# Kernel tuning notes

Hardware: AMD Instinct MI355X
Metric: run time of the kernel (lower is better)

## Reference

```python
import jax, jax.numpy as jnp
import numpy as np

B, H, S = 2048, 1024, 128


def setup_inputs() -> dict:
    key = jax.random.key(0)
    ks = jax.random.split(key, 8)
    s = 0.05  # keep gates out of saturation, roughly 1/sqrt(H) init scale
    return {
        "hidden": jax.random.normal(ks[0], (1, B, H), jnp.float32) * s,
        "cell": jax.random.normal(ks[1], (1, B, H), jnp.float32) * s,
        "W_ih": jax.random.normal(ks[2], (4 * H, 1), jnp.float32) * s,
        "W_hh": jax.random.normal(ks[3], (4 * H, H), jnp.float32) * s,
        "b_ih": jax.random.normal(ks[4], (4 * H,), jnp.float32) * s,
        "b_hh": jax.random.normal(ks[5], (4 * H,), jnp.float32) * s,
        "W_fc": jax.random.normal(ks[6], (S, H), jnp.float32) * s,
        "b_fc": jax.random.normal(ks[7], (S,), jnp.float32) * s,
    }


def reference(hidden, cell, W_ih, W_hh, b_ih, b_hh, W_fc, b_fc):
    # prediction from per-step head fc_i fed back as next input.
    h0 = hidden[0]  # [B, H] (num_layers = 1)
    c0 = cell[0]
    b = b_ih + b_hh  # [4H]
    x0 = jnp.zeros((h0.shape[0], 1), h0.dtype)  # initial zero input [B, 1]

    def step(carry, fc_t):
        h, c, x = carry
        Wt, bt = fc_t  # Wt: [H], bt: scalar
        gates = x @ W_ih.T + h @ W_hh.T + b  # [B, 4H], torch gate order i,f,g,o
        i, f, g, o = jnp.split(gates, 4, axis=-1)
        c = jax.nn.sigmoid(f) * c + jax.nn.sigmoid(i) * jnp.tanh(g)
        h = jax.nn.sigmoid(o) * jnp.tanh(c)
        pred = h @ Wt + bt  # [B] (Linear(H,1) then squeeze)
        return (h, c, pred[:, None]), pred

    _, preds = jax.lax.scan(step, (h0, c0, x0), (W_fc, b_fc))  # preds: [S, B]
    return preds.T  # [B, S]
```

## Files before the change

kernel.cpp:

```cpp
#include <hip/hip_runtime.h>
#include <hip/hip_bf16.h>
#include <stdint.h>

#define B_SZ 2048
#define H_SZ 1024
#define S_SZ 128
#define G4   4096
#define BK   64
#define NKK  (H_SZ / BK)

typedef short short8 __attribute__((ext_vector_type(8)));
typedef float floatx4 __attribute__((ext_vector_type(4)));

#define AS1 __attribute__((address_space(1)))
#define AS3 __attribute__((address_space(3)))

__device__ ushort g_Wp[G4 * H_SZ];
__device__ ushort g_h[2][B_SZ * H_SZ];
__device__ float  g_c[B_SZ * H_SZ];
__device__ float  g_wih[G4];
__device__ float  g_bias[G4];
__device__ float  g_pp[2][32][B_SZ];

__device__ __forceinline__ float bf2f(ushort u) {
  return __uint_as_float(((unsigned)u) << 16);
}
__device__ __forceinline__ ushort f2bf(float f) {
  unsigned u = __float_as_uint(f);
  return (ushort)((u + 0x7FFFu + ((u >> 16) & 1u)) >> 16);
}
__device__ __forceinline__ float fsig(float x) { return 1.f / (1.f + __expf(-x)); }
__device__ __forceinline__ float ftanh(float x) { return 1.f - 2.f / (__expf(2.f * x) + 1.f); }

__device__ __forceinline__ void gload16(const void* g, void* l) {
  __builtin_amdgcn_global_load_lds((const AS1 void*)g, (AS3 void*)l, 16, 0, 0);
}


__global__ __launch_bounds__(256) void prep_wpack(const float* __restrict__ Whh) {
  const int gid = blockIdx.x * 256 + threadIdx.x;
  const int j   = gid >> 7;
  const int k8  = (gid & 127) << 3;
  const int gate = (j >> 4) & 3;
  const int h    = ((j >> 6) << 4) | (j & 15);
  const float* src = Whh + (size_t)(gate * H_SZ + h) * H_SZ + k8;
  floatx4 a = *(const floatx4*)src;
  floatx4 b = *(const floatx4*)(src + 4);
  short8 o;
#pragma unroll
  for (int i = 0; i < 4; ++i) o[i] = (short)f2bf(a[i]);
#pragma unroll
  for (int i = 0; i < 4; ++i) o[4 + i] = (short)f2bf(b[i]);
  *(short8*)&g_Wp[(size_t)j * H_SZ + (k8 ^ ((j & 7) << 3))] = o;
}

__global__ __launch_bounds__(256) void prep_misc(const float* __restrict__ Wih,
                                                 const float* __restrict__ bih,
                                                 const float* __restrict__ bhh) {
  const int j = blockIdx.x * 256 + threadIdx.x;
  const int gate = (j >> 4) & 3;
  const int h    = ((j >> 6) << 4) | (j & 15);
  const int jp   = gate * H_SZ + h;
  g_wih[j]  = Wih[jp];
  g_bias[j] = bih[jp] + bhh[jp];
}

__global__ __launch_bounds__(256) void prep_state(const float* __restrict__ hidden,
                                                  const float* __restrict__ cell) {
  const int gid = blockIdx.x * 256 + threadIdx.x;
  const int row = gid >> 7;
  const int k8  = (gid & 127) << 3;
  const size_t src = (size_t)row * H_SZ + k8;
  short8 o;
#pragma unroll
  for (int i = 0; i < 8; ++i) o[i] = (short)f2bf(hidden[src + i]);
  *(short8*)&g_h[0][(size_t)row * H_SZ + (k8 ^ ((row & 7) << 3))] = o;
  floatx4 c0 = *(const floatx4*)&cell[src];
  floatx4 c1 = *(const floatx4*)&cell[src + 4];
  *(floatx4*)&g_c[src]     = c0;
  *(floatx4*)&g_c[src + 4] = c1;
}

__global__ __launch_bounds__(256, 2)
void lstm_step(int t, int p, const float* __restrict__ Wfc,
               const float* __restrict__ bfc, float* __restrict__ out) {
  __shared__ ushort Al[2][128 * BK];
  __shared__ ushort Bl[2][128 * BK];

  const ushort* __restrict__ hin = g_h[p];
  ushort* __restrict__ hout      = g_h[p ^ 1];

  const int tid  = threadIdx.x;
  const int lane = tid & 63;
  const int wid  = tid >> 6;
  const int bid  = blockIdx.x;
  const int xcd  = bid & 7;
  const int idx  = bid >> 3;
  const int jt   = (xcd << 2) | (idx & 3);
  const int bt   = idx >> 2;
  const int brow = bt << 7;
  const int jcol = jt << 7;
  const int wr = wid >> 1, wc = wid & 1;
  const int lr = lane & 15, lk = lane >> 4;
  const int xorv = (lr & 7) << 3;

  const int srow = lane >> 3;
  const int scol = (lane & 7) << 3;
  const size_t arb = (size_t)(brow + wid * 32 + srow) * H_SZ + scol;
  const size_t brb = (size_t)(jcol + wid * 32 + srow) * H_SZ + scol;
  ushort* const ad0 = &Al[0][wid * 32 * BK];
  ushort* const ad1 = &Al[1][wid * 32 * BK];
  ushort* const bd0 = &Bl[0][wid * 32 * BK];
  ushort* const bd1 = &Bl[1][wid * 32 * BK];

  floatx4 acc[4][4];
#pragma unroll
  for (int m = 0; m < 4; ++m)
#pragma unroll
    for (int n = 0; n < 4; ++n) acc[m][n] = {0.f, 0.f, 0.f, 0.f};

  int aoff[4], boff[4];
#pragma unroll
  for (int m = 0; m < 4; ++m) aoff[m] = (wr * 64 + m * 16 + lr) * BK;
#pragma unroll
  for (int n = 0; n < 4; ++n) boff[n] = (wc * 64 + n * 16 + lr) * BK;
  const int c0 = (lk * 8) ^ xorv;
  const int c1 = (32 + lk * 8) ^ xorv;

#define STAGE(AD, BD, KO)                                                   \
  {                                                                         \
    const int ko_ = (KO) * BK;                                              \
    _Pragma("unroll") for (int i = 0; i < 4; ++i) {                         \
      gload16(hin + arb + (size_t)i * 8 * H_SZ + ko_, AD + i * 8 * BK);     \
      gload16(g_Wp + brb + (size_t)i * 8 * H_SZ + ko_, BD + i * 8 * BK);    \
    }                                                                       \
  }

#define COMPUTE(AC, BC)                                                     \
  {                                                                         \
    short8 a[4], b[4];                                                      \
    _Pragma("unroll") for (int k2 = 0; k2 < 2; ++k2) {                      \
      const int cc_ = k2 ? c1 : c0;                                         \
      _Pragma("unroll") for (int m = 0; m < 4; ++m)                         \
          a[m] = *(const short8*)&(AC)[aoff[m] + cc_];                      \
      _Pragma("unroll") for (int n = 0; n < 4; ++n)                         \
          b[n] = *(const short8*)&(BC)[boff[n] + cc_];                      \
      _Pragma("unroll") for (int m = 0; m < 4; ++m)                         \
          _Pragma("unroll") for (int n = 0; n < 4; ++n)                     \
              acc[m][n] = __builtin_amdgcn_mfma_f32_16x16x32_bf16(          \
                  a[m], b[n], acc[m][n], 0, 0, 0);                          \
    }                                                                       \
  }

  STAGE(ad0, bd0, 0);
  __syncthreads();

  for (int kk = 0; kk < NKK; kk += 2) {
    STAGE(ad1, bd1, kk + 1);
    COMPUTE(Al[0], Bl[0]);
    __syncthreads();
    if (kk + 2 < NKK) STAGE(ad0, bd0, kk + 2);
    COMPUTE(Al[1], Bl[1]);
    __syncthreads();
  }

  float* predp = (float*)&Al[0][0];
  float* xbuf  = (float*)&Bl[0][0];

  if (t > 0 && tid < 128) {
    float s = 0.f;
#pragma unroll
    for (int j = 0; j < 32; ++j) s += g_pp[(t - 1) & 1][j][brow + tid];
    s += bfc[t - 1];
    xbuf[tid] = s;
    if (jt == 0) out[(size_t)(brow + tid) * S_SZ + (t - 1)] = s;
  }
  __syncthreads();

  const int hcol = ((jt * 2 + wc) << 4) + lr;
  const float wfc_l = Wfc[(size_t)t * H_SZ + hcol];
  float wih[4], bb[4];
#pragma unroll
  for (int n = 0; n < 4; ++n) {
    const int col = jcol + wc * 64 + n * 16 + lr;
    wih[n] = g_wih[col];
    bb[n]  = g_bias[col];
  }

#pragma unroll
  for (int m = 0; m < 4; ++m) {
#pragma unroll
    for (int r = 0; r < 4; ++r) {
      const int row_l = wr * 64 + m * 16 + lk * 4 + r;
      const float xv = (t > 0) ? xbuf[row_l] : 0.f;
      float gi = acc[m][0][r] + xv * wih[0] + bb[0];
      float gf = acc[m][1][r] + xv * wih[1] + bb[1];
      float gg = acc[m][2][r] + xv * wih[2] + bb[2];
      float go = acc[m][3][r] + xv * wih[3] + bb[3];
      const int row = brow + row_l;
      const size_t cidx = (size_t)row * H_SZ + hcol;
      float cc = g_c[cidx];
      float cn = fsig(gf) * cc + fsig(gi) * ftanh(gg);
      g_c[cidx] = cn;
      float hv = fsig(go) * ftanh(cn);
      hout[(size_t)row * H_SZ + (hcol ^ ((row_l & 7) << 3))] = f2bf(hv);
      float pp = hv * wfc_l;
      pp += __shfl_xor(pp, 1);
      pp += __shfl_xor(pp, 2);
      pp += __shfl_xor(pp, 4);
      pp += __shfl_xor(pp, 8);
      if (lr == 0) predp[wc * 128 + row_l] = pp;
    }
  }
  __syncthreads();
  if (tid < 128) g_pp[t & 1][jt][brow + tid] = predp[tid] + predp[128 + tid];
#undef STAGE
#undef COMPUTE
}

__global__ __launch_bounds__(256)
void pred_last(const float* __restrict__ bfc, float* __restrict__ out) {
  const int row = blockIdx.x * 256 + threadIdx.x;
  float s = 0.f;
#pragma unroll
  for (int j = 0; j < 32; ++j) s += g_pp[1][j][row];
  out[(size_t)row * S_SZ + (S_SZ - 1)] = s + bfc[S_SZ - 1];
}

extern "C" void kernel_launch(void* const* d_in, const int* in_sizes, int n_in,
                              void* d_out, int out_size, void* d_ws, size_t ws_size,
                              hipStream_t stream) {
  const float* hidden = (const float*)d_in[0];
  const float* cell   = (const float*)d_in[1];
  const float* W_ih   = (const float*)d_in[2];
  const float* W_hh   = (const float*)d_in[3];
  const float* b_ih   = (const float*)d_in[4];
  const float* b_hh   = (const float*)d_in[5];
  const float* W_fc   = (const float*)d_in[6];
  const float* b_fc   = (const float*)d_in[7];
  float* out = (float*)d_out;

  prep_wpack<<<2048, 256, 0, stream>>>(W_hh);
  prep_misc<<<16, 256, 0, stream>>>(W_ih, b_ih, b_hh);
  prep_state<<<1024, 256, 0, stream>>>(hidden, cell);

  for (int t = 0; t < S_SZ; ++t) {
    lstm_step<<<512, 256, 0, stream>>>(t, t & 1, W_fc, b_fc, out);
  }
  pred_last<<<8, 256, 0, stream>>>(b_fc, out);
}
```

Baseline: 4.818 ms.

## Fuse all LSTM timesteps into one persistent kernel with grid barrier

Replaces the 128 per-timestep kernel launches with a single persistent kernel of 256 blocks of 512 threads. Blocks synchronise between timesteps through a hierarchical atomic grid barrier. The cell state now stays in registers across steps instead of being read from and written to global memory. The tile shape also changes to 128x256 with BK=32 and a 4-way XOR swizzle. The persistent design depends on all 256 blocks being co-resident for the spin barrier to avoid deadlock, and the smaller BK tiles mean more barriers per step.

```diff
diff --git a/kernel.cpp b/kernel.cpp
--- a/kernel.cpp
+++ b/kernel.cpp
@@ -6,8 +6,12 @@
 #define H_SZ 1024
 #define S_SZ 128
 #define G4   4096
-#define BK   64
+#define BK   32
 #define NKK  (H_SZ / BK)
+#define BM   128
+#define BN   256
+#define NJT  16
+#define NBLK 256
 
 typedef short short8 __attribute__((ext_vector_type(8)));
 typedef float floatx4 __attribute__((ext_vector_type(4)));
@@ -17,10 +21,12 @@
 
 __device__ ushort g_Wp[G4 * H_SZ];
 __device__ ushort g_h[2][B_SZ * H_SZ];
-__device__ float  g_c[B_SZ * H_SZ];
 __device__ float  g_wih[G4];
 __device__ float  g_bias[G4];
-__device__ float  g_pp[2][32][B_SZ];
+__device__ float  g_pp[2][NJT][B_SZ];
+__device__ unsigned g_leaf[8 * 32];
+__device__ unsigned g_root;
+__device__ unsigned g_gen;
 
 __device__ __forceinline__ float bf2f(ushort u) {
   return __uint_as_float(((unsigned)u) << 16);
@@ -34,6 +40,33 @@
 
 __device__ __forceinline__ void gload16(const void* g, void* l) {
   __builtin_amdgcn_global_load_lds((const AS1 void*)g, (AS3 void*)l, 16, 0, 0);
+}
+
+__device__ __forceinline__ void grid_barrier(int grp) {
+  __syncthreads();
+  if (threadIdx.x == 0) {
+    __threadfence();
+    unsigned gen = __hip_atomic_load(&g_gen, __ATOMIC_RELAXED, __HIP_MEMORY_SCOPE_AGENT);
+    unsigned a = __hip_atomic_fetch_add(&g_leaf[grp * 32], 1u, __ATOMIC_ACQ_REL,
+                                        __HIP_MEMORY_SCOPE_AGENT);
+    if (a == 31u) {
+      __hip_atomic_store(&g_leaf[grp * 32], 0u, __ATOMIC_RELAXED, __HIP_MEMORY_SCOPE_AGENT);
+      unsigned r = __hip_atomic_fetch_add(&g_root, 1u, __ATOMIC_ACQ_REL,
+                                          __HIP_MEMORY_SCOPE_AGENT);
+      if (r == 7u) {
+        __hip_atomic_store(&g_root, 0u, __ATOMIC_RELAXED, __HIP_MEMORY_SCOPE_AGENT);
+        __hip_atomic_store(&g_gen, gen + 1u, __ATOMIC_RELEASE, __HIP_MEMORY_SCOPE_AGENT);
+      } else {
+        while (__hip_atomic_load(&g_gen, __ATOMIC_RELAXED, __HIP_MEMORY_SCOPE_AGENT) == gen)
+          __builtin_amdgcn_s_sleep(2);
+      }
+    } else {
+      while (__hip_atomic_load(&g_gen, __ATOMIC_RELAXED, __HIP_MEMORY_SCOPE_AGENT) == gen)
+        __builtin_amdgcn_s_sleep(2);
+    }
+    __threadfence();
+  }
+  __syncthreads();
 }
 
 
@@ -51,12 +84,16 @@
   for (int i = 0; i < 4; ++i) o[i] = (short)f2bf(a[i]);
 #pragma unroll
   for (int i = 0; i < 4; ++i) o[4 + i] = (short)f2bf(b[i]);
-  *(short8*)&g_Wp[(size_t)j * H_SZ + (k8 ^ ((j & 7) << 3))] = o;
+  *(short8*)&g_Wp[(size_t)j * H_SZ + (k8 ^ ((j & 3) << 3))] = o;
 }
 
 __global__ __launch_bounds__(256) void prep_misc(const float* __restrict__ Wih,
                                                  const float* __restrict__ bih,
                                                  const float* __restrict__ bhh) {
+  if (blockIdx.x == 0) {
+    if (threadIdx.x == 0) { g_root = 0u; g_gen = 0u; }
+    if (threadIdx.x < 8) g_leaf[threadIdx.x * 32] = 0u;
+  }
   const int j = blockIdx.x * 256 + threadIdx.x;
   const int gate = (j >> 4) & 3;
   const int h    = ((j >> 6) << 4) | (j & 15);
@@ -65,8 +102,7 @@
   g_bias[j] = bih[jp] + bhh[jp];
 }
 
-__global__ __launch_bounds__(256) void prep_state(const float* __restrict__ hidden,
-                                                  const float* __restrict__ cell) {
+__global__ __launch_bounds__(256) void prep_h(const float* __restrict__ hidden) {
   const int gid = blockIdx.x * 256 + threadIdx.x;
   const int row = gid >> 7;
   const int k8  = (gid & 127) << 3;
@@ -74,111 +110,46 @@
   short8 o;
 #pragma unroll
   for (int i = 0; i < 8; ++i) o[i] = (short)f2bf(hidden[src + i]);
-  *(short8*)&g_h[0][(size_t)row * H_SZ + (k8 ^ ((row & 7) << 3))] = o;
-  floatx4 c0 = *(const floatx4*)&cell[src];
-  floatx4 c1 = *(const floatx4*)&cell[src + 4];
-  *(floatx4*)&g_c[src]     = c0;
-  *(floatx4*)&g_c[src + 4] = c1;
-}
-
-__global__ __launch_bounds__(256, 2)
-void lstm_step(int t, int p, const float* __restrict__ Wfc,
-               const float* __restrict__ bfc, float* __restrict__ out) {
-  __shared__ ushort Al[2][128 * BK];
-  __shared__ ushort Bl[2][128 * BK];
-
-  const ushort* __restrict__ hin = g_h[p];
-  ushort* __restrict__ hout      = g_h[p ^ 1];
+  *(short8*)&g_h[0][(size_t)row * H_SZ + (k8 ^ ((row & 3) << 3))] = o;
+}
+
+__global__ __launch_bounds__(512, 2)
+void lstm_persistent(const float* __restrict__ cell,
+                     const float* __restrict__ Wfc,
+                     const float* __restrict__ bfc,
+                     float* __restrict__ out) {
+  __shared__ ushort Al[2][BM * BK];
+  __shared__ ushort Bl[2][BN * BK];
+  __shared__ float  xbuf[BM];
+  __shared__ float  predp[4 * BM];
 
   const int tid  = threadIdx.x;
   const int lane = tid & 63;
   const int wid  = tid >> 6;
   const int bid  = blockIdx.x;
-  const int xcd  = bid & 7;
+  const int grp  = bid & 7;
   const int idx  = bid >> 3;
-  const int jt   = (xcd << 2) | (idx & 3);
-  const int bt   = idx >> 2;
-  const int brow = bt << 7;
-  const int jcol = jt << 7;
-  const int wr = wid >> 1, wc = wid & 1;
+  const int jt   = (grp & 3) * 4 + (idx & 3);
+  const int bt   = (grp >> 2) * 8 + (idx >> 2);
+  const int brow = bt * BM;
+  const int jcol = jt * BN;
+  const int wr = wid >> 2, wc = wid & 3;
   const int lr = lane & 15, lk = lane >> 4;
-  const int xorv = (lr & 7) << 3;
-
-  const int srow = lane >> 3;
-  const int scol = (lane & 7) << 3;
-  const size_t arb = (size_t)(brow + wid * 32 + srow) * H_SZ + scol;
-  const size_t brb = (size_t)(jcol + wid * 32 + srow) * H_SZ + scol;
-  ushort* const ad0 = &Al[0][wid * 32 * BK];
-  ushort* const ad1 = &Al[1][wid * 32 * BK];
-  ushort* const bd0 = &Bl[0][wid * 32 * BK];
-  ushort* const bd1 = &Bl[1][wid * 32 * BK];
-
-  floatx4 acc[4][4];
-#pragma unroll
-  for (int m = 0; m < 4; ++m)
-#pragma unroll
-    for (int n = 0; n < 4; ++n) acc[m][n] = {0.f, 0.f, 0.f, 0.f};
+
+  const int srow   = wid * 16 + (lane >> 2);
+  const int schunk = (lane & 3) << 3;
+  const size_t abase  = (size_t)(brow + srow) * H_SZ + schunk;
+  const size_t bbase0 = (size_t)(jcol + srow) * H_SZ + schunk;
+  const size_t bbase1 = bbase0 + (size_t)128 * H_SZ;
 
   int aoff[4], boff[4];
 #pragma unroll
   for (int m = 0; m < 4; ++m) aoff[m] = (wr * 64 + m * 16 + lr) * BK;
 #pragma unroll
   for (int n = 0; n < 4; ++n) boff[n] = (wc * 64 + n * 16 + lr) * BK;
-  const int c0 = (lk * 8) ^ xorv;
-  const int c1 = (32 + lk * 8) ^ xorv;
-
-#define STAGE(AD, BD, KO)                                                   \
-  {                                                                         \
-    const int ko_ = (KO) * BK;                                              \
-    _Pragma("unroll") for (int i = 0; i < 4; ++i) {                         \
-      gload16(hin + arb + (size_t)i * 8 * H_SZ + ko_, AD + i * 8 * BK);     \
-      gload16(g_Wp + brb + (size_t)i * 8 * H_SZ + ko_, BD + i * 8 * BK);    \
-    }                                                                       \
-  }
-
-#define COMPUTE(AC, BC)                                                     \
-  {                                                                         \
-    short8 a[4], b[4];                                                      \
-    _Pragma("unroll") for (int k2 = 0; k2 < 2; ++k2) {                      \
-      const int cc_ = k2 ? c1 : c0;                                         \
-      _Pragma("unroll") for (int m = 0; m < 4; ++m)                         \
-          a[m] = *(const short8*)&(AC)[aoff[m] + cc_];                      \
-      _Pragma("unroll") for (int n = 0; n < 4; ++n)                         \
-          b[n] = *(const short8*)&(BC)[boff[n] + cc_];                      \
-      _Pragma("unroll") for (int m = 0; m < 4; ++m)                         \
-          _Pragma("unroll") for (int n = 0; n < 4; ++n)                     \
-              acc[m][n] = __builtin_amdgcn_mfma_f32_16x16x32_bf16(          \
-                  a[m], b[n], acc[m][n], 0, 0, 0);                          \
-    }                                                                       \
-  }
-
-  STAGE(ad0, bd0, 0);
-  __syncthreads();
-
-  for (int kk = 0; kk < NKK; kk += 2) {
-    STAGE(ad1, bd1, kk + 1);
-    COMPUTE(Al[0], Bl[0]);
-    __syncthreads();
-    if (kk + 2 < NKK) STAGE(ad0, bd0, kk + 2);
-    COMPUTE(Al[1], Bl[1]);
-    __syncthreads();
-  }
-
-  float* predp = (float*)&Al[0][0];
-  float* xbuf  = (float*)&Bl[0][0];
-
-  if (t > 0 && tid < 128) {
-    float s = 0.f;
-#pragma unroll
-    for (int j = 0; j < 32; ++j) s += g_pp[(t - 1) & 1][j][brow + tid];
-    s += bfc[t - 1];
-    xbuf[tid] = s;
-    if (jt == 0) out[(size_t)(brow + tid) * S_SZ + (t - 1)] = s;
-  }
-  __syncthreads();
-
-  const int hcol = ((jt * 2 + wc) << 4) + lr;
-  const float wfc_l = Wfc[(size_t)t * H_SZ + hcol];
+  const int cc = (lk * 8) ^ ((lr & 3) << 3);
+
+  const int hcol = jt * 64 + wc * 16 + lr;
   float wih[4], bb[4];
 #pragma unroll
   for (int n = 0; n < 4; ++n) {
@@ -187,44 +158,109 @@
     bb[n]  = g_bias[col];
   }
 
-#pragma unroll
-  for (int m = 0; m < 4; ++m) {
+  float creg[4][4];
+#pragma unroll
+  for (int m = 0; m < 4; ++m)
 #pragma unroll
     for (int r = 0; r < 4; ++r) {
       const int row_l = wr * 64 + m * 16 + lk * 4 + r;
-      const float xv = (t > 0) ? xbuf[row_l] : 0.f;
-      float gi = acc[m][0][r] + xv * wih[0] + bb[0];
-      float gf = acc[m][1][r] + xv * wih[1] + bb[1];
-      float gg = acc[m][2][r] + xv * wih[2] + bb[2];
-      float go = acc[m][3][r] + xv * wih[3] + bb[3];
-      const int row = brow + row_l;
-      const size_t cidx = (size_t)row * H_SZ + hcol;
-      float cc = g_c[cidx];
-      float cn = fsig(gf) * cc + fsig(gi) * ftanh(gg);
-      g_c[cidx] = cn;
-      float hv = fsig(go) * ftanh(cn);
-      hout[(size_t)row * H_SZ + (hcol ^ ((row_l & 7) << 3))] = f2bf(hv);
-      float pp = hv * wfc_l;
-      pp += __shfl_xor(pp, 1);
-      pp += __shfl_xor(pp, 2);
-      pp += __shfl_xor(pp, 4);
-      pp += __shfl_xor(pp, 8);
-      if (lr == 0) predp[wc * 128 + row_l] = pp;
-    }
-  }
-  __syncthreads();
-  if (tid < 128) g_pp[t & 1][jt][brow + tid] = predp[tid] + predp[128 + tid];
+      creg[m][r] = cell[(size_t)(brow + row_l) * H_SZ + hcol];
+    }
+
+#define STAGE(BUF, KO)                                                      \
+  {                                                                         \
+    const int ko_ = (KO) * BK;                                              \
+    gload16(hin + abase + ko_, &Al[BUF][wid * 512]);                        \
+    gload16(g_Wp + bbase0 + ko_, &Bl[BUF][wid * 512]);                      \
+    gload16(g_Wp + bbase1 + ko_, &Bl[BUF][4096 + wid * 512]);               \
+  }
+
+#define COMPUTE(BUF)                                                        \
+  {                                                                         \
+    short8 a[4], b[4];                                                      \
+    _Pragma("unroll") for (int m = 0; m < 4; ++m)                           \
+        a[m] = *(const short8*)&Al[BUF][aoff[m] + cc];                      \
+    _Pragma("unroll") for (int n = 0; n < 4; ++n)                           \
+        b[n] = *(const short8*)&Bl[BUF][boff[n] + cc];                      \
+    _Pragma("unroll") for (int m = 0; m < 4; ++m)                           \
+        _Pragma("unroll") for (int n = 0; n < 4; ++n)                       \
+            acc[m][n] = __builtin_amdgcn_mfma_f32_16x16x32_bf16(            \
+                a[m], b[n], acc[m][n], 0, 0, 0);                            \
+  }
+
+  for (int t = 0; t < S_SZ; ++t) {
+    const int p = t & 1;
+    const ushort* __restrict__ hin = g_h[p];
+    ushort* __restrict__ hout      = g_h[p ^ 1];
+
+    floatx4 acc[4][4];
+#pragma unroll
+    for (int m = 0; m < 4; ++m)
+#pragma unroll
+      for (int n = 0; n < 4; ++n) acc[m][n] = {0.f, 0.f, 0.f, 0.f};
+
+    STAGE(0, 0);
+    __syncthreads();
+
+    for (int kk = 0; kk < NKK; kk += 2) {
+      STAGE(1, kk + 1);
+      COMPUTE(0);
+      __syncthreads();
+      if (kk + 2 < NKK) STAGE(0, kk + 2);
+      COMPUTE(1);
+      __syncthreads();
+    }
+
+    if (t > 0 && tid < BM) {
+      float s = 0.f;
+#pragma unroll
+      for (int j = 0; j < NJT; ++j) s += g_pp[(t - 1) & 1][j][brow + tid];
+      s += bfc[t - 1];
+      xbuf[tid] = s;
+      if (jt == 0) out[(size_t)(brow + tid) * S_SZ + (t - 1)] = s;
+    }
+    __syncthreads();
+
+    const float wfc_l = Wfc[(size_t)t * H_SZ + hcol];
+
+#pragma unroll
+    for (int m = 0; m < 4; ++m) {
+#pragma unroll
+      for (int r = 0; r < 4; ++r) {
+        const int row_l = wr * 64 + m * 16 + lk * 4 + r;
+        const float xv = (t > 0) ? xbuf[row_l] : 0.f;
+        float gi = acc[m][0][r] + xv * wih[0] + bb[0];
+        float gf = acc[m][1][r] + xv * wih[1] + bb[1];
+        float gg = acc[m][2][r] + xv * wih[2] + bb[2];
+        float go = acc[m][3][r] + xv * wih[3] + bb[3];
+        float cn = fsig(gf) * creg[m][r] + fsig(gi) * ftanh(gg);
+        creg[m][r] = cn;
+        float hv = fsig(go) * ftanh(cn);
+        hout[(size_t)(brow + row_l) * H_SZ + (hcol ^ (r << 3))] = f2bf(hv);
+        float pp = hv * wfc_l;
+        pp += __shfl_xor(pp, 1);
+        pp += __shfl_xor(pp, 2);
+        pp += __shfl_xor(pp, 4);
+        pp += __shfl_xor(pp, 8);
+        if (lr == 0) predp[wc * BM + row_l] = pp;
+      }
+    }
+    __syncthreads();
+    if (tid < BM)
+      g_pp[p][jt][brow + tid] = predp[tid] + predp[BM + tid] +
+                                predp[2 * BM + tid] + predp[3 * BM + tid];
+
+    grid_barrier(grp);
+  }
+
+  if (jt == 0 && tid < BM) {
+    float s = 0.f;
+#pragma unroll
+    for (int j = 0; j < NJT; ++j) s += g_pp[1][j][brow + tid];
+    out[(size_t)(brow + tid) * S_SZ + (S_SZ - 1)] = s + bfc[S_SZ - 1];
+  }
 #undef STAGE
 #undef COMPUTE
-}
-
-__global__ __launch_bounds__(256)
-void pred_last(const float* __restrict__ bfc, float* __restrict__ out) {
-  const int row = blockIdx.x * 256 + threadIdx.x;
-  float s = 0.f;
-#pragma unroll
-  for (int j = 0; j < 32; ++j) s += g_pp[1][j][row];
-  out[(size_t)row * S_SZ + (S_SZ - 1)] = s + bfc[S_SZ - 1];
 }
 
 extern "C" void kernel_launch(void* const* d_in, const int* in_sizes, int n_in,
@@ -242,10 +278,7 @@
 
   prep_wpack<<<2048, 256, 0, stream>>>(W_hh);
   prep_misc<<<16, 256, 0, stream>>>(W_ih, b_ih, b_hh);
-  prep_state<<<1024, 256, 0, stream>>>(hidden, cell);
-
-  for (int t = 0; t < S_SZ; ++t) {
-    lstm_step<<<512, 256, 0, stream>>>(t, t & 1, W_fc, b_fc, out);
-  }
-  pred_last<<<8, 256, 0, stream>>>(b_fc, out);
-}
+  prep_h<<<1024, 256, 0, stream>>>(hidden);
+
+  lstm_persistent<<<NBLK, 512, 0, stream>>>(cell, W_fc, b_fc, out);
+}
```

After: 7.102 ms. 47.4% more time.
